# Kernel optimization log

Measured on AMD Instinct MI355X. Metric: run time of the kernel, lower is better.

The kernel has to match this reference:

```python
import jax, jax.numpy as jnp
import numpy as np
from jax import lax

B, H, W = 8, 500, 500
M = 2048          # per-image cap on active bottleneck voxels (ragged -> fixed)
GRID = 125        # bottleneck grid size
ENC_RANGE = 125.0
HEADS, ATTN_CH, CH = 4, 128, 64
EPS = 1e-5
NEG = -1e9

def _conv(x, w, b, stride, pad):
    y = lax.conv_general_dilated(x, w, (stride, stride), pad,
                                 dimension_numbers=('NCHW', 'HWIO', 'NCHW'))
    return y + b[None, :, None, None]

def _maxpool2(m):
    return lax.reduce_window(m, -jnp.inf, lax.max, (1, 1, 2, 2), (1, 1, 2, 2), 'VALID')

def setup_inputs():
    key = jax.random.key(0)
    ks = jax.random.split(key, 12)
    occ = (jax.random.uniform(ks[0], (B, 1, H, W)) < 0.005).astype(jnp.float32)
    x = jax.random.normal(ks[1], (B, 1, H, W), dtype=jnp.float32) * occ
    def rn(k, shape, scale):
        return jax.random.normal(k, shape, dtype=jnp.float32) * scale
    return {
        'x': x,
        'w0': rn(ks[2], (3, 3, 1, 32), 0.3), 'b0': jnp.zeros(32, jnp.float32),
        'g0': jnp.ones(32, jnp.float32), 'be0': jnp.zeros(32, jnp.float32),
        'w1': rn(ks[3], (2, 2, 32, 64), 0.1), 'b1': jnp.zeros(64, jnp.float32),
        'g1': jnp.ones(64, jnp.float32), 'be1': jnp.zeros(64, jnp.float32),
        'w2': rn(ks[4], (2, 2, 64, 64), 0.08), 'b2': jnp.zeros(64, jnp.float32),
        'g2': jnp.ones(64, jnp.float32), 'be2': jnp.zeros(64, jnp.float32),
        'wpe': rn(ks[5], (2, 2, CH), 0.5), 'bpe': jnp.zeros((2, CH), jnp.float32),
        'wq': rn(ks[6], (2, CH, ATTN_CH), 0.12), 'bq': jnp.zeros((2, ATTN_CH), jnp.float32),
        'wk': rn(ks[7], (2, CH, ATTN_CH), 0.12), 'bk': jnp.zeros((2, ATTN_CH), jnp.float32),
        'wv': rn(ks[8], (2, CH, ATTN_CH), 0.12), 'bv': jnp.zeros((2, ATTN_CH), jnp.float32),
        'wo': rn(ks[9], (2, ATTN_CH, CH), 0.09), 'bo': jnp.zeros((2, CH), jnp.float32),
        'wh': rn(ks[10], (CH, 4), 0.12), 'bh': jnp.zeros(4, jnp.float32),
    }

def reference(x, w0, b0, g0, be0, w1, b1, g1, be1, w2, b2, g2, be2,
              wpe, bpe, wq, bq, wk, bk, wv, bv, wo, bo, wh, bh):
    # active-site mask (Voxels.from_dense)
    mask0 = (x != 0).any(axis=1, keepdims=True).astype(x.dtype)   # [B,1,500,500]

    def bn_relu(y, g, be):
        # eval-mode BatchNorm1d over active voxel features (running stats 0/1)
        return jax.nn.relu(g[None, :, None, None] * y / jnp.sqrt(1.0 + EPS)
                           + be[None, :, None, None])

    # enc0: submanifold 3x3/s1 -> active set unchanged; inactive inputs are zero
    y = bn_relu(_conv(x, w0, b0, 1, 'SAME'), g0, be0) * mask0
    # enc1/enc2: strided 2x2/s2 -> output active iff any input in window active
    mask1 = _maxpool2(mask0)
    y = bn_relu(_conv(y, w1, b1, 2, 'VALID'), g1, be1) * mask1
    mask2 = _maxpool2(mask1)
    y = bn_relu(_conv(y, w2, b2, 2, 'VALID'), g2, be2) * mask2    # [B,64,125,125]

    # gather active bottleneck voxels per image (ragged -> fixed M + validity mask)
    mflat = mask2.reshape(B, GRID * GRID)
    vals, idx = lax.top_k(mflat, M)     # active-first; stable tie-break (lowest idx)
    valid = vals                        # [B,M] in {0,1}
    feats = jnp.take_along_axis(
        y.reshape(B, CH, GRID * GRID).transpose(0, 2, 1),
        idx[:, :, None], axis=1)        # [B,M,64]
    pos = jnp.stack([idx // GRID, idx % GRID], axis=-1).astype(x.dtype) / ENC_RANGE

    dh = ATTN_CH // HEADS
    kmask = (1.0 - valid)[:, None, None, :] * NEG
    for i in range(2):  # N_ATTN structurally distinct layers
        pe = pos @ wpe[i] + bpe[i]
        h = feats + pe
        q = (h @ wq[i] + bq[i]).reshape(B, M, HEADS, dh)
        k = (h @ wk[i] + bk[i]).reshape(B, M, HEADS, dh)
        v = (h @ wv[i] + bv[i]).reshape(B, M, HEADS, dh)
        s = jnp.einsum('bqhd,bkhd->bhqk', q, k) / jnp.sqrt(jnp.asarray(dh, x.dtype))
        a = jax.nn.softmax(s + kmask, axis=-1)
        o = jnp.einsum('bhqk,bkhd->bqhd', a, v).reshape(B, M, ATTN_CH)
        feats = (feats + o @ wo[i] + bo[i]) * valid[..., None]

    # sparse_global_avg_pool: mean over active voxels per image
    counts = jnp.clip(valid.sum(axis=1, keepdims=True), 1.0, None)
    pooled = feats.sum(axis=1) / counts                            # [B,64]
    return pooled @ wh + bh                                        # [B,4]
```

## Files before the change

kernel.cpp:

```cpp
#include <hip/hip_runtime.h>

#define BDIM   8
#define NPIX   250000
#define G1N    62500
#define G2N    15625
#define NB0    977
#define NB1    245
#define NB2    62
#define NBALL  (NB0 + NB1 + NB2)
#define CAP0   4096
#define CAP1   4096
#define CAPM   2048
#define CH     64
#define ACH    128
#define NHEADS 4
#define DH     32
#define KSPLIT 4

static constexpr float BN_INV = 0.99999500003749969f;
static constexpr float SCALE2 = 0.25505654734044769f;

typedef _Float16 f16x8 __attribute__((ext_vector_type(8)));
typedef __fp16 h16x2 __attribute__((ext_vector_type(2)));
typedef float f32x4 __attribute__((ext_vector_type(4)));

static constexpr size_t E_MAP0  = 0;
static constexpr size_t E_MAP1  = E_MAP0 + (size_t)BDIM*NPIX;
static constexpr size_t E_CNT   = E_MAP1 + (size_t)BDIM*G1N;
static constexpr size_t E_ZEND  = E_CNT + 32;
static constexpr size_t E_BC    = E_ZEND;
static constexpr size_t E_BO    = E_BC + (size_t)3*BDIM*1024;
static constexpr size_t E_BM    = E_BO + (size_t)3*BDIM*1024;
static constexpr size_t E_LIST0 = E_BM + (size_t)3*BDIM*1024*8;
static constexpr size_t E_LIST1 = E_LIST0 + (size_t)BDIM*CAP0;
static constexpr size_t E_LIST2 = E_LIST1 + (size_t)BDIM*CAP1;
static constexpr size_t E_Y0    = E_LIST2 + (size_t)BDIM*CAPM;
static constexpr size_t E_Y1    = E_Y0 + (size_t)BDIM*CAP0*32;
static constexpr size_t E_FE    = E_Y1 + (size_t)BDIM*CAP1*64;
static constexpr size_t E_QF    = E_FE + (size_t)BDIM*CAPM*64;
static constexpr size_t E_KF    = E_QF + (size_t)32*CAPM*32/2;
static constexpr size_t E_VT    = E_KF + (size_t)32*CAPM*32/2;
static constexpr size_t E_O     = E_VT + (size_t)32*CAPM*32/2;


__global__ __launch_bounds__(256) void k_cntA(const float* __restrict__ x,
                                              int* __restrict__ bcnt,
                                              unsigned long long* __restrict__ bm) {
  int bx = blockIdx.x, b = blockIdx.y, tid = threadIdx.x;
  int level, blk;
  bool act = false;
  if (bx < NB0) {
    level = 0; blk = bx;
    int idx = blk * 256 + tid;
    act = (idx < NPIX) && (x[(size_t)b * NPIX + idx] != 0.f);
  } else if (bx < NB0 + NB1) {
    level = 1; blk = bx - NB0;
    int p = blk * 256 + tid;
    if (p < G1N) {
      int i = p / 250, j = p - i * 250;
      const float* px = x + (size_t)b * NPIX + (2 * i) * 500 + 2 * j;
      act = (px[0] != 0.f) | (px[1] != 0.f) | (px[500] != 0.f) | (px[501] != 0.f);
    }
  } else {
    level = 2; blk = bx - NB0 - NB1;
    int p = blk * 256 + tid;
    if (p < G2N) {
      int i = p / 125, j = p - i * 125;
      const float* px = x + (size_t)b * NPIX + (4 * i) * 500 + 4 * j;
      bool a = false;
#pragma unroll
      for (int r = 0; r < 4; ++r)
#pragma unroll
        for (int c = 0; c < 4; ++c) a |= (px[r * 500 + c] != 0.f);
      act = a;
    }
  }
  unsigned long long mask = __ballot(act);
  size_t mbase = ((size_t)level * BDIM + b) * 1024 + blk;
  __shared__ int wc[4];
  if ((tid & 63) == 0) {
    wc[tid >> 6] = __popcll(mask);
    bm[mbase * 4 + (tid >> 6)] = mask;
  }
  __syncthreads();
  if (tid == 0) bcnt[mbase] = wc[0] + wc[1] + wc[2] + wc[3];
}

__global__ __launch_bounds__(256) void k_emitA(
    const unsigned long long* __restrict__ bm, const int* __restrict__ bcnt,
    int* __restrict__ map0, int* __restrict__ list0,
    int* __restrict__ map1, int* __restrict__ list1,
    int* __restrict__ list2, int* __restrict__ cnt) {
  int bx = blockIdx.x, b = blockIdx.y, tid = threadIdx.x;
  int level, blk, nblk, cbase;
  if (bx < NB0)            { level = 0; blk = bx;             nblk = NB0; cbase = 0; }
  else if (bx < NB0 + NB1) { level = 1; blk = bx - NB0;       nblk = NB1; cbase = BDIM; }
  else                     { level = 2; blk = bx - NB0 - NB1; nblk = NB2; cbase = 2 * BDIM; }
  size_t mbase = ((size_t)level * BDIM + b) * 1024;
  int lane = tid & 63, wv = tid >> 6;
  unsigned long long mask = bm[(mbase + blk) * 4 + wv];
  const int* bc = bcnt + mbase;
  int pre = 0;
  for (int k = tid; k < blk; k += 256) pre += bc[k];
#pragma unroll
  for (int off = 1; off < 64; off <<= 1) pre += __shfl_xor(pre, off);
  __shared__ int wred[4], wbase[4];
  if (lane == 0) { wred[wv] = pre; wbase[wv] = __popcll(mask); }
  __syncthreads();
  if (tid == 0) {
    int s = wred[0] + wred[1] + wred[2] + wred[3];
    for (int w = 0; w < 4; ++w) { int c = wbase[w]; wbase[w] = s; s += c; }
    if (blk == nblk - 1) cnt[cbase + b] = s;
  }
  __syncthreads();
  bool act = (mask >> lane) & 1;
  int slot = wbase[wv] + __popcll(mask & ((1ull << lane) - 1ull));
  int idx = blk * 256 + tid;
  if (level == 0) {
    if (act && slot < CAP0) {
      list0[b * CAP0 + slot] = idx;
      map0[(size_t)b * NPIX + idx] = slot + 1;
    }
  } else if (level == 1) {
    if (act && slot < CAP1) {
      list1[b * CAP1 + slot] = idx;
      map1[(size_t)b * G1N + idx] = slot + 1;
    }
  } else {
    if (act && slot < CAPM) list2[b * CAPM + slot] = idx;
  }
}


__global__ void k_y0(const float* __restrict__ x, const float* __restrict__ w0,
                     const float* __restrict__ b0, const float* __restrict__ g0,
                     const float* __restrict__ be0,
                     const int* __restrict__ list0, const int* __restrict__ cnt,
                     float* __restrict__ y0) {
  int t = blockIdx.x * 256 + threadIdx.x;
  int b = t >> 17;
  int r = t & 131071;
  int slot = r >> 5, c = r & 31;
  int n = min(cnt[b], CAP0);
  if (slot >= n) return;
  int pix = list0[b * CAP0 + slot];
  int i = pix / 500, j = pix - i * 500;
  float acc = b0[c];
#pragma unroll
  for (int di = 0; di < 3; ++di) {
    int ii = i + di - 1;
    if ((unsigned)ii >= 500u) continue;
#pragma unroll
    for (int dj = 0; dj < 3; ++dj) {
      int jj = j + dj - 1;
      if ((unsigned)jj >= 500u) continue;
      acc += x[(size_t)b * NPIX + ii * 500 + jj] * w0[(di * 3 + dj) * 32 + c];
    }
  }
  float o = g0[c] * acc * BN_INV + be0[c];
  y0[((size_t)(b * CAP0) + slot) * 32 + c] = fmaxf(o, 0.f);
}

__global__ __launch_bounds__(256) void k_y1(
    const float* __restrict__ y0, const float* __restrict__ w1,
    const float* __restrict__ b1, const float* __restrict__ g1,
    const float* __restrict__ be1,
    const int* __restrict__ map0, const int* __restrict__ list1,
    const int* __restrict__ cnt, float* __restrict__ y1) {
  int b = blockIdx.x & 7;
  int qblk = blockIdx.x >> 3;
  int sub = threadIdx.x >> 6;
  int co = threadIdx.x & 63;
  int n = min(cnt[BDIM + b], CAP1);
  if (qblk * 32 >= n) return;
  int s0 = qblk * 32 + sub * 8;
  __shared__ float inT[4][4][32][8];
  for (int idx = co; idx < 1024; idx += 64) {
    int s = idx & 7;
    int r = idx >> 3;
    int ci = r & 31, pp = r >> 5;
    float v = 0.f;
    int sg = s0 + s;
    if (sg < n) {
      int p = list1[b * CAP1 + sg];
      int i = p / 250, j = p - i * 250;
      int sm = map0[(size_t)b * NPIX + (2 * i + (pp >> 1)) * 500 + (2 * j + (pp & 1))];
      if (sm) v = y0[((size_t)(b * CAP0) + (sm - 1)) * 32 + ci];
    }
    inT[sub][pp][ci][s] = v;
  }
  __syncthreads();
  float acc[8];
#pragma unroll
  for (int s = 0; s < 8; ++s) acc[s] = b1[co];
#pragma unroll 2
  for (int pp = 0; pp < 4; ++pp)
    for (int ci = 0; ci < 32; ++ci) {
      float wv = w1[((pp << 5) + ci) * 64 + co];
      float4 i0 = *(const float4*)&inT[sub][pp][ci][0];
      float4 i1 = *(const float4*)&inT[sub][pp][ci][4];
      acc[0] += i0.x * wv; acc[1] += i0.y * wv; acc[2] += i0.z * wv; acc[3] += i0.w * wv;
      acc[4] += i1.x * wv; acc[5] += i1.y * wv; acc[6] += i1.z * wv; acc[7] += i1.w * wv;
    }
  int smax = min(8, n - s0);
  for (int s = 0; s < smax; ++s) {
    float o = g1[co] * acc[s] * BN_INV + be1[co];
    y1[((size_t)(b * CAP1) + s0 + s) * 64 + co] = fmaxf(o, 0.f);
  }
}

__global__ __launch_bounds__(256) void k_y2(
    const float* __restrict__ y1, const float* __restrict__ w2,
    const float* __restrict__ b2, const float* __restrict__ g2,
    const float* __restrict__ be2,
    const int* __restrict__ map1, const int* __restrict__ list2,
    const int* __restrict__ cnt, float* __restrict__ feats) {
  int b = blockIdx.x & 7;
  int qblk = blockIdx.x >> 3;
  int sub = threadIdx.x >> 6;
  int co = threadIdx.x & 63;
  int n = min(cnt[2 * BDIM + b], CAPM);
  if (qblk * 32 >= n) return;
  int s0 = qblk * 32 + sub * 8;
  __shared__ float inT[4][4][64][8];
  for (int idx = co; idx < 2048; idx += 64) {
    int s = idx & 7;
    int r = idx >> 3;
    int ci = r & 63, pp = r >> 6;
    float v = 0.f;
    int sg = s0 + s;
    if (sg < n) {
      int p = list2[b * CAPM + sg];
      int i = p / 125, j = p - i * 125;
      int sm = map1[(size_t)b * G1N + (2 * i + (pp >> 1)) * 250 + (2 * j + (pp & 1))];
      if (sm) v = y1[((size_t)(b * CAP1) + (sm - 1)) * 64 + ci];
    }
    inT[sub][pp][ci][s] = v;
  }
  __syncthreads();
  float acc[8];
#pragma unroll
  for (int s = 0; s < 8; ++s) acc[s] = b2[co];
#pragma unroll 2
  for (int pp = 0; pp < 4; ++pp)
    for (int ci = 0; ci < 64; ++ci) {
      float wv = w2[((pp << 6) + ci) * 64 + co];
      float4 i0 = *(const float4*)&inT[sub][pp][ci][0];
      float4 i1 = *(const float4*)&inT[sub][pp][ci][4];
      acc[0] += i0.x * wv; acc[1] += i0.y * wv; acc[2] += i0.z * wv; acc[3] += i0.w * wv;
      acc[4] += i1.x * wv; acc[5] += i1.y * wv; acc[6] += i1.z * wv; acc[7] += i1.w * wv;
    }
  int smax = min(8, n - s0);
  for (int s = 0; s < smax; ++s) {
    float o = g2[co] * acc[s] * BN_INV + be2[co];
    feats[((size_t)(b * CAPM) + s0 + s) * 64 + co] = fmaxf(o, 0.f);
  }
}


__global__ __launch_bounds__(256) void k_qkv(
    const float* __restrict__ feats, const int* __restrict__ list2,
    const int* __restrict__ cnt,
    const float* __restrict__ wpe, const float* __restrict__ bpe,
    const float* __restrict__ wq, const float* __restrict__ bq,
    const float* __restrict__ wk, const float* __restrict__ bk,
    const float* __restrict__ wv, const float* __restrict__ bv,
    int layer, _Float16* __restrict__ qf, _Float16* __restrict__ kf,
    _Float16* __restrict__ vt) {
  int b = blockIdx.x & 7;
  int qblk = blockIdx.x >> 3;
  int sub = threadIdx.x >> 7;
  int o = threadIdx.x & 127;
  int n = min(cnt[2 * BDIM + b], CAPM);
  if (qblk * 16 >= n) return;
  int s0 = qblk * 16 + sub * 8;
  __shared__ float hT[2][64][8];
  for (int idx = o; idx < 512; idx += 128) {
    int s = idx & 7, c = idx >> 3;
    float hv = 0.f;
    int sg = s0 + s;
    if (sg < n) {
      int p = list2[b * CAPM + sg];
      int i = p / 125, j = p - i * 125;
      hv = feats[((size_t)(b * CAPM) + sg) * 64 + c]
         + (float)i * (1.f / 125.f) * wpe[(layer * 2 + 0) * 64 + c]
         + (float)j * (1.f / 125.f) * wpe[(layer * 2 + 1) * 64 + c]
         + bpe[layer * 64 + c];
    }
    hT[sub][c][s] = hv;
  }
  __syncthreads();
  float accq[8], acck[8], accv[8];
  float bqv = bq[layer * 128 + o], bkv = bk[layer * 128 + o], bvv = bv[layer * 128 + o];
#pragma unroll
  for (int s = 0; s < 8; ++s) { accq[s] = bqv; acck[s] = bkv; accv[s] = bvv; }
  const float* wq_ = wq + (size_t)layer * 64 * 128 + o;
  const float* wk_ = wk + (size_t)layer * 64 * 128 + o;
  const float* wv_ = wv + (size_t)layer * 64 * 128 + o;
  for (int c = 0; c < 64; ++c) {
    float wqv = wq_[c * 128], wkv = wk_[c * 128], wvv = wv_[c * 128];
    float4 h0 = *(const float4*)&hT[sub][c][0];
    float4 h1 = *(const float4*)&hT[sub][c][4];
    float hh[8] = {h0.x, h0.y, h0.z, h0.w, h1.x, h1.y, h1.z, h1.w};
#pragma unroll
    for (int s = 0; s < 8; ++s) {
      accq[s] += hh[s] * wqv; acck[s] += hh[s] * wkv; accv[s] += hh[s] * wvv;
    }
  }
  int hd = o >> 5, d = o & 31;
  size_t bh = (size_t)(b * NHEADS + hd);
  int smax = min(8, n - s0);
  for (int s = 0; s < smax; ++s) {
    size_t rb = (bh * CAPM + s0 + s) * 32 + d;
    qf[rb] = (_Float16)(accq[s] * SCALE2);
    kf[rb] = (_Float16)acck[s];
    vt[(bh * 32 + d) * CAPM + s0 + s] = (_Float16)accv[s];
  }
}


union U4H8 { uint4 u; f16x8 h; };
union PK2  { h16x2 h; unsigned int u; };

__device__ __forceinline__ void ptile(
    f16x8 K0, f16x8 K1, f16x8 K2, f16x8 K3,
    f16x8 V0, f16x8 V1, f16x8 V2, f16x8 V3,
    f16x8 fq, f32x4& acc0, f32x4& acc1, float& m, float& l, bool& first,
    unsigned int* P, int swz, int g, int qr, int n, int T0) {
  f32x4 cm = { -m, -m, -m, -m };
  f32x4 st0 = __builtin_amdgcn_mfma_f32_16x16x32_f16(K0, fq, cm, 0, 0, 0);
  f32x4 st1 = __builtin_amdgcn_mfma_f32_16x16x32_f16(K1, fq, cm, 0, 0, 0);
  f32x4 st2 = __builtin_amdgcn_mfma_f32_16x16x32_f16(K2, fq, cm, 0, 0, 0);
  f32x4 st3 = __builtin_amdgcn_mfma_f32_16x16x32_f16(K3, fq, cm, 0, 0, 0);
  if (T0 + 64 > n) {
#pragma unroll
    for (int r = 0; r < 4; ++r) {
      if (T0 + 4 * g + r >= n)      st0[r] = -1e30f;
      if (T0 + 16 + 4 * g + r >= n) st1[r] = -1e30f;
      if (T0 + 32 + 4 * g + r >= n) st2[r] = -1e30f;
      if (T0 + 48 + 4 * g + r >= n) st3[r] = -1e30f;
    }
  }
  float x0 = fmaxf(fmaxf(st0[0], st0[1]), st0[2]);
  float x1 = fmaxf(fmaxf(st0[3], st1[0]), st1[1]);
  float x2 = fmaxf(fmaxf(st1[2], st1[3]), st2[0]);
  float x3 = fmaxf(fmaxf(st2[1], st2[2]), st2[3]);
  float x4 = fmaxf(fmaxf(st3[0], st3[1]), st3[2]);
  float tm = fmaxf(fmaxf(fmaxf(x0, x1), fmaxf(x2, x3)), fmaxf(x4, st3[3]));
  tm = fmaxf(tm, __shfl_xor(tm, 16));
  tm = fmaxf(tm, __shfl_xor(tm, 32));
  bool gw = first || (__any(tm > 0.f) != 0);
  float d = 0.f;
  if (gw) {
    d = first ? tm : fmaxf(tm, 0.f);
    if (!first) {
      float f_ = exp2f(-d);
      l *= f_;
      acc0 *= f_;
      acc1 *= f_;
    }
    m += d;
    first = false;
  }
  PK2 a0, a1, a2, a3, a4, a5, a6, a7;
  a0.h = __builtin_amdgcn_cvt_pkrtz(exp2f(st0[0] - d), exp2f(st0[1] - d));
  a1.h = __builtin_amdgcn_cvt_pkrtz(exp2f(st0[2] - d), exp2f(st0[3] - d));
  a2.h = __builtin_amdgcn_cvt_pkrtz(exp2f(st1[0] - d), exp2f(st1[1] - d));
  a3.h = __builtin_amdgcn_cvt_pkrtz(exp2f(st1[2] - d), exp2f(st1[3] - d));
  a4.h = __builtin_amdgcn_cvt_pkrtz(exp2f(st2[0] - d), exp2f(st2[1] - d));
  a5.h = __builtin_amdgcn_cvt_pkrtz(exp2f(st2[2] - d), exp2f(st2[3] - d));
  a6.h = __builtin_amdgcn_cvt_pkrtz(exp2f(st3[0] - d), exp2f(st3[1] - d));
  a7.h = __builtin_amdgcn_cvt_pkrtz(exp2f(st3[2] - d), exp2f(st3[3] - d));
  h16x2 one2 = { (__fp16)1.f, (__fp16)1.f };
  float ls = 0.f;
  ls = __builtin_amdgcn_fdot2(a0.h, one2, ls, false);
  ls = __builtin_amdgcn_fdot2(a1.h, one2, ls, false);
  ls = __builtin_amdgcn_fdot2(a2.h, one2, ls, false);
  ls = __builtin_amdgcn_fdot2(a3.h, one2, ls, false);
  ls = __builtin_amdgcn_fdot2(a4.h, one2, ls, false);
  ls = __builtin_amdgcn_fdot2(a5.h, one2, ls, false);
  ls = __builtin_amdgcn_fdot2(a6.h, one2, ls, false);
  ls = __builtin_amdgcn_fdot2(a7.h, one2, ls, false);
  l += ls;
  P[(qr * 32 + 0 + 2 * g) ^ swz] = a0.u;
  P[(qr * 32 + 1 + 2 * g) ^ swz] = a1.u;
  P[(qr * 32 + 8 + 2 * g) ^ swz] = a2.u;
  P[(qr * 32 + 9 + 2 * g) ^ swz] = a3.u;
  P[(qr * 32 + 16 + 2 * g) ^ swz] = a4.u;
  P[(qr * 32 + 17 + 2 * g) ^ swz] = a5.u;
  P[(qr * 32 + 24 + 2 * g) ^ swz] = a6.u;
  P[(qr * 32 + 25 + 2 * g) ^ swz] = a7.u;
  __builtin_amdgcn_sched_barrier(0);
  U4H8 pa0, pa1;
  pa0.u = *(const uint4*)&P[(qr * 32 + 4 * g) ^ swz];
  pa1.u = *(const uint4*)&P[(qr * 32 + 16 + 4 * g) ^ swz];
  acc0 = __builtin_amdgcn_mfma_f32_16x16x32_f16(V0, pa0.h, acc0, 0, 0, 0);
  acc1 = __builtin_amdgcn_mfma_f32_16x16x32_f16(V1, pa0.h, acc1, 0, 0, 0);
  acc0 = __builtin_amdgcn_mfma_f32_16x16x32_f16(V2, pa1.h, acc0, 0, 0, 0);
  acc1 = __builtin_amdgcn_mfma_f32_16x16x32_f16(V3, pa1.h, acc1, 0, 0, 0);
}

#define LOADK(K0, K1, K2, K3, T0)                                          \
  K0 = *(const f16x8*)(kf + (bh + (T0) + qr) * 32 + g8);                   \
  K1 = *(const f16x8*)(kf + (bh + (T0) + 16 + qr) * 32 + g8);              \
  K2 = *(const f16x8*)(kf + (bh + (T0) + 32 + qr) * 32 + g8);              \
  K3 = *(const f16x8*)(kf + (bh + (T0) + 48 + qr) * 32 + g8);

#define LOADV(V0, V1, V2, V3, T0)                                          \
  V0 = *(const f16x8*)(vbase + (size_t)qr * CAPM + (T0) + g8);             \
  V1 = *(const f16x8*)(vbase + (size_t)(16 + qr) * CAPM + (T0) + g8);      \
  V2 = *(const f16x8*)(vbase + (size_t)qr * CAPM + (T0) + 32 + g8);        \
  V3 = *(const f16x8*)(vbase + (size_t)(16 + qr) * CAPM + (T0) + 32 + g8);

__global__ __launch_bounds__(256) void k_attn(
    const _Float16* __restrict__ qf, const _Float16* __restrict__ kf,
    const _Float16* __restrict__ vt, const int* __restrict__ cnt,
    _Float16* __restrict__ obuf) {
  int b  = blockIdx.x & 7;
  int rr = blockIdx.x >> 3;
  int qt = rr & 127;
  int h  = rr >> 7;
  int n = min(cnt[2 * BDIM + b], CAPM);
  int q0 = qt * 16;
  if (q0 >= n) return;
  int ks = threadIdx.x >> 6;
  int lane = threadIdx.x & 63;
  int g = lane >> 4, qr = lane & 15;
  int g8 = g * 8;
  size_t bh = (size_t)(b * NHEADS + h) * CAPM;
  const _Float16* vbase = vt + (size_t)(b * NHEADS + h) * 32 * CAPM;
  f16x8 fq = *(const f16x8*)(qf + (bh + q0 + qr) * 32 + g8);
  f32x4 acc0 = {0.f, 0.f, 0.f, 0.f}, acc1 = {0.f, 0.f, 0.f, 0.f};
  float m = 0.f, l = 0.f;
  bool first = true;
  __shared__ unsigned int P4[4][512];
  __shared__ float partA[4][16][33];
  __shared__ float mlA[4][16][2];
  unsigned int* P = P4[ks];
  int swz = (qr & 7) << 2;

  int nt = (n + 63) >> 6;
  int tpc = (nt + KSPLIT - 1) / KSPLIT;
  int tb = ks * tpc, te = min(nt, tb + tpc);
  if (tb < te) {
    f16x8 ka0, ka1, ka2, ka3, va0, va1, va2, va3;
    f16x8 kb0, kb1, kb2, kb3, vb0, vb1, vb2, vb3;
    LOADK(ka0, ka1, ka2, ka3, tb * 64)
    LOADV(va0, va1, va2, va3, tb * 64)
    for (int t = tb; t < te; t += 2) {
      if (t + 1 < te) {
        LOADK(kb0, kb1, kb2, kb3, (t + 1) * 64)
        LOADV(vb0, vb1, vb2, vb3, (t + 1) * 64)
      }
      ptile(ka0, ka1, ka2, ka3, va0, va1, va2, va3, fq, acc0, acc1, m, l,
            first, P, swz, g, qr, n, t * 64);
      if (t + 1 < te) {
        if (t + 2 < te) {
          LOADK(ka0, ka1, ka2, ka3, (t + 2) * 64)
          LOADV(va0, va1, va2, va3, (t + 2) * 64)
        }
        ptile(kb0, kb1, kb2, kb3, vb0, vb1, vb2, vb3, fq, acc0, acc1, m, l,
              first, P, swz, g, qr, n, (t + 1) * 64);
      }
    }
  }
  l += __shfl_xor(l, 16);
  l += __shfl_xor(l, 32);
#pragma unroll
  for (int r = 0; r < 4; ++r) {
    partA[ks][qr][4 * g + r] = acc0[r];
    partA[ks][qr][16 + 4 * g + r] = acc1[r];
  }
  if (g == 0) { mlA[ks][qr][0] = first ? -1e30f : m; mlA[ks][qr][1] = l; }
  __syncthreads();
  int t = threadIdx.x;
  int s = t >> 4;
  int c0 = (t & 15) * 2;
  int tok = q0 + s;
  if (tok < n) {
    float m0 = mlA[0][s][0], l0 = mlA[0][s][1];
    float m1 = mlA[1][s][0], l1 = mlA[1][s][1];
    float m2 = mlA[2][s][0], l2 = mlA[2][s][1];
    float m3 = mlA[3][s][0], l3 = mlA[3][s][1];
    float M = fmaxf(fmaxf(m0, m1), fmaxf(m2, m3));
    float w0_ = exp2f(m0 - M), w1_ = exp2f(m1 - M);
    float w2_ = exp2f(m2 - M), w3_ = exp2f(m3 - M);
    float invL = 1.f / (w0_ * l0 + w1_ * l1 + w2_ * l2 + w3_ * l3);
    float v0 = (partA[0][s][c0] * w0_ + partA[1][s][c0] * w1_ +
                partA[2][s][c0] * w2_ + partA[3][s][c0] * w3_) * invL;
    float v1 = (partA[0][s][c0 + 1] * w0_ + partA[1][s][c0 + 1] * w1_ +
                partA[2][s][c0 + 1] * w2_ + partA[3][s][c0 + 1] * w3_) * invL;
    _Float16* op = obuf + ((size_t)b * CAPM + tok) * ACH + h * DH;
    op[c0] = (_Float16)v0;
    op[c0 + 1] = (_Float16)v1;
  }
}


__global__ __launch_bounds__(256) void k_proj(
    const _Float16* __restrict__ obuf, const float* __restrict__ wo,
    const float* __restrict__ bo, const int* __restrict__ cnt,
    int layer, float* __restrict__ feats) {
  int b = blockIdx.x & 7;
  int sblk = blockIdx.x >> 3;
  int s0 = sblk * 4;
  int n = min(cnt[2 * BDIM + b], CAPM);
  if (s0 >= n) return;
  __shared__ float oT[128][4];
  int t = threadIdx.x;
#pragma unroll
  for (int k = 0; k < 2; ++k) {
    int id = t + k * 256;
    int c = id >> 2, s = id & 3;
    int sg = s0 + s;
    oT[c][s] = (sg < n) ? (float)obuf[((size_t)b * CAPM + sg) * ACH + c] : 0.f;
  }
  __syncthreads();
  int s = t >> 6, co = t & 63;
  float acc = bo[layer * 64 + co];
  const float* w = wo + (size_t)layer * 128 * 64 + co;
#pragma unroll 8
  for (int c = 0; c < 128; ++c) acc += oT[c][s] * w[c * 64];
  int tok = s0 + s;
  if (tok < n) feats[((size_t)(b * CAPM) + tok) * 64 + co] += acc;
}


__global__ __launch_bounds__(1024) void k_head(
    const float* __restrict__ feats, const float* __restrict__ wh,
    const float* __restrict__ bhd, const int* __restrict__ cnt,
    float* __restrict__ out) {
  int b = blockIdx.x;
  int n = min(cnt[2 * BDIM + b], CAPM);
  int c = threadIdx.x & 63, chunk = threadIdx.x >> 6;
  int lo = chunk * 128, hi = min(n, lo + 128);
  float s = 0.f;
  for (int mm = lo; mm < hi; ++mm)
    s += feats[((size_t)(b * CAPM) + mm) * 64 + c];
  __shared__ float red[16][64];
  __shared__ float pooled[64];
  red[chunk][c] = s;
  __syncthreads();
  if (threadIdx.x < 64) {
    float tot = 0.f;
#pragma unroll
    for (int k = 0; k < 16; ++k) tot += red[k][c];
    pooled[c] = tot / (float)max(n, 1);
  }
  __syncthreads();
  if (threadIdx.x < 4) {
    float o = bhd[threadIdx.x];
#pragma unroll
    for (int c2 = 0; c2 < 64; ++c2) o += pooled[c2] * wh[c2 * 4 + threadIdx.x];
    out[b * 4 + threadIdx.x] = o;
  }
}


extern "C" void kernel_launch(void* const* d_in, const int* in_sizes, int n_in,
                              void* d_out, int out_size, void* d_ws, size_t ws_size,
                              hipStream_t stream) {
  const float* x   = (const float*)d_in[0];
  const float* w0  = (const float*)d_in[1];
  const float* b0  = (const float*)d_in[2];
  const float* g0  = (const float*)d_in[3];
  const float* be0 = (const float*)d_in[4];
  const float* w1  = (const float*)d_in[5];
  const float* b1  = (const float*)d_in[6];
  const float* g1  = (const float*)d_in[7];
  const float* be1 = (const float*)d_in[8];
  const float* w2  = (const float*)d_in[9];
  const float* b2  = (const float*)d_in[10];
  const float* g2  = (const float*)d_in[11];
  const float* be2 = (const float*)d_in[12];
  const float* wpe = (const float*)d_in[13];
  const float* bpe = (const float*)d_in[14];
  const float* wq  = (const float*)d_in[15];
  const float* bq  = (const float*)d_in[16];
  const float* wk  = (const float*)d_in[17];
  const float* bk  = (const float*)d_in[18];
  const float* wv  = (const float*)d_in[19];
  const float* bv  = (const float*)d_in[20];
  const float* wo  = (const float*)d_in[21];
  const float* bo  = (const float*)d_in[22];
  const float* wh  = (const float*)d_in[23];
  const float* bh  = (const float*)d_in[24];

  int* wsI = (int*)d_ws;
  float* wsF = (float*)d_ws;
  unsigned long long* bm = (unsigned long long*)(wsI + E_BM);
  _Float16* qf = (_Float16*)(wsI + E_QF);
  _Float16* kf = (_Float16*)(wsI + E_KF);
  _Float16* vt = (_Float16*)(wsI + E_VT);
  _Float16* ob = (_Float16*)(wsI + E_O);

  hipMemsetAsync(d_ws, 0, E_ZEND * 4, stream);

  k_cntA<<<dim3(NBALL, BDIM), 256, 0, stream>>>(x, wsI + E_BC, bm);
  k_emitA<<<dim3(NBALL, BDIM), 256, 0, stream>>>(
      bm, wsI + E_BC, wsI + E_MAP0, wsI + E_LIST0, wsI + E_MAP1, wsI + E_LIST1,
      wsI + E_LIST2, wsI + E_CNT);

  k_y0<<<(BDIM * CAP0 * 32) / 256, 256, 0, stream>>>(
      x, w0, b0, g0, be0, wsI + E_LIST0, wsI + E_CNT, wsF + E_Y0);
  k_y1<<<BDIM * (CAP1 / 32), 256, 0, stream>>>(
      wsF + E_Y0, w1, b1, g1, be1, wsI + E_MAP0, wsI + E_LIST1, wsI + E_CNT, wsF + E_Y1);
  k_y2<<<BDIM * (CAPM / 32), 256, 0, stream>>>(
      wsF + E_Y1, w2, b2, g2, be2, wsI + E_MAP1, wsI + E_LIST2, wsI + E_CNT, wsF + E_FE);

  for (int layer = 0; layer < 2; ++layer) {
    k_qkv<<<BDIM * (CAPM / 16), 256, 0, stream>>>(
        wsF + E_FE, wsI + E_LIST2, wsI + E_CNT, wpe, bpe, wq, bq, wk, bk, wv, bv,
        layer, qf, kf, vt);
    k_attn<<<BDIM * NHEADS * (CAPM / 16), 256, 0, stream>>>(
        qf, kf, vt, wsI + E_CNT, ob);
    k_proj<<<BDIM * (CAPM / 4), 256, 0, stream>>>(
        ob, wo, bo, wsI + E_CNT, layer, wsF + E_FE);
  }

  k_head<<<BDIM, 1024, 0, stream>>>(wsF + E_FE, wh, bh, wsI + E_CNT, (float*)d_out);
}
```

Baseline: 239.1 us.

## Software-pipeline QK^T MFMAs one tile ahead of softmax in attention kernel

Splits the per-tile attention step into a QK^T stage and a softmax/PV stage. The loop now issues the score MFMAs for the next key tile before running the exp/rowsum/PV work of the current one, so matrix-core latency can overlap with VALU work. It also reworks the online-softmax bookkeeping: the max starts at -1e30 and is subtracted explicitly instead of being folded into the MFMA accumulator, and the `first` flag and a sched_barrier are removed. The price is more live score registers, which may raise register pressure.

```diff
diff --git a/kernel.cpp b/kernel.cpp
--- a/kernel.cpp
+++ b/kernel.cpp
@@ -322,84 +322,6 @@
 union U4H8 { uint4 u; f16x8 h; };
 union PK2  { h16x2 h; unsigned int u; };
 
-__device__ __forceinline__ void ptile(
-    f16x8 K0, f16x8 K1, f16x8 K2, f16x8 K3,
-    f16x8 V0, f16x8 V1, f16x8 V2, f16x8 V3,
-    f16x8 fq, f32x4& acc0, f32x4& acc1, float& m, float& l, bool& first,
-    unsigned int* P, int swz, int g, int qr, int n, int T0) {
-  f32x4 cm = { -m, -m, -m, -m };
-  f32x4 st0 = __builtin_amdgcn_mfma_f32_16x16x32_f16(K0, fq, cm, 0, 0, 0);
-  f32x4 st1 = __builtin_amdgcn_mfma_f32_16x16x32_f16(K1, fq, cm, 0, 0, 0);
-  f32x4 st2 = __builtin_amdgcn_mfma_f32_16x16x32_f16(K2, fq, cm, 0, 0, 0);
-  f32x4 st3 = __builtin_amdgcn_mfma_f32_16x16x32_f16(K3, fq, cm, 0, 0, 0);
-  if (T0 + 64 > n) {
-#pragma unroll
-    for (int r = 0; r < 4; ++r) {
-      if (T0 + 4 * g + r >= n)      st0[r] = -1e30f;
-      if (T0 + 16 + 4 * g + r >= n) st1[r] = -1e30f;
-      if (T0 + 32 + 4 * g + r >= n) st2[r] = -1e30f;
-      if (T0 + 48 + 4 * g + r >= n) st3[r] = -1e30f;
-    }
-  }
-  float x0 = fmaxf(fmaxf(st0[0], st0[1]), st0[2]);
-  float x1 = fmaxf(fmaxf(st0[3], st1[0]), st1[1]);
-  float x2 = fmaxf(fmaxf(st1[2], st1[3]), st2[0]);
-  float x3 = fmaxf(fmaxf(st2[1], st2[2]), st2[3]);
-  float x4 = fmaxf(fmaxf(st3[0], st3[1]), st3[2]);
-  float tm = fmaxf(fmaxf(fmaxf(x0, x1), fmaxf(x2, x3)), fmaxf(x4, st3[3]));
-  tm = fmaxf(tm, __shfl_xor(tm, 16));
-  tm = fmaxf(tm, __shfl_xor(tm, 32));
-  bool gw = first || (__any(tm > 0.f) != 0);
-  float d = 0.f;
-  if (gw) {
-    d = first ? tm : fmaxf(tm, 0.f);
-    if (!first) {
-      float f_ = exp2f(-d);
-      l *= f_;
-      acc0 *= f_;
-      acc1 *= f_;
-    }
-    m += d;
-    first = false;
-  }
-  PK2 a0, a1, a2, a3, a4, a5, a6, a7;
-  a0.h = __builtin_amdgcn_cvt_pkrtz(exp2f(st0[0] - d), exp2f(st0[1] - d));
-  a1.h = __builtin_amdgcn_cvt_pkrtz(exp2f(st0[2] - d), exp2f(st0[3] - d));
-  a2.h = __builtin_amdgcn_cvt_pkrtz(exp2f(st1[0] - d), exp2f(st1[1] - d));
-  a3.h = __builtin_amdgcn_cvt_pkrtz(exp2f(st1[2] - d), exp2f(st1[3] - d));
-  a4.h = __builtin_amdgcn_cvt_pkrtz(exp2f(st2[0] - d), exp2f(st2[1] - d));
-  a5.h = __builtin_amdgcn_cvt_pkrtz(exp2f(st2[2] - d), exp2f(st2[3] - d));
-  a6.h = __builtin_amdgcn_cvt_pkrtz(exp2f(st3[0] - d), exp2f(st3[1] - d));
-  a7.h = __builtin_amdgcn_cvt_pkrtz(exp2f(st3[2] - d), exp2f(st3[3] - d));
-  h16x2 one2 = { (__fp16)1.f, (__fp16)1.f };
-  float ls = 0.f;
-  ls = __builtin_amdgcn_fdot2(a0.h, one2, ls, false);
-  ls = __builtin_amdgcn_fdot2(a1.h, one2, ls, false);
-  ls = __builtin_amdgcn_fdot2(a2.h, one2, ls, false);
-  ls = __builtin_amdgcn_fdot2(a3.h, one2, ls, false);
-  ls = __builtin_amdgcn_fdot2(a4.h, one2, ls, false);
-  ls = __builtin_amdgcn_fdot2(a5.h, one2, ls, false);
-  ls = __builtin_amdgcn_fdot2(a6.h, one2, ls, false);
-  ls = __builtin_amdgcn_fdot2(a7.h, one2, ls, false);
-  l += ls;
-  P[(qr * 32 + 0 + 2 * g) ^ swz] = a0.u;
-  P[(qr * 32 + 1 + 2 * g) ^ swz] = a1.u;
-  P[(qr * 32 + 8 + 2 * g) ^ swz] = a2.u;
-  P[(qr * 32 + 9 + 2 * g) ^ swz] = a3.u;
-  P[(qr * 32 + 16 + 2 * g) ^ swz] = a4.u;
-  P[(qr * 32 + 17 + 2 * g) ^ swz] = a5.u;
-  P[(qr * 32 + 24 + 2 * g) ^ swz] = a6.u;
-  P[(qr * 32 + 25 + 2 * g) ^ swz] = a7.u;
-  __builtin_amdgcn_sched_barrier(0);
-  U4H8 pa0, pa1;
-  pa0.u = *(const uint4*)&P[(qr * 32 + 4 * g) ^ swz];
-  pa1.u = *(const uint4*)&P[(qr * 32 + 16 + 4 * g) ^ swz];
-  acc0 = __builtin_amdgcn_mfma_f32_16x16x32_f16(V0, pa0.h, acc0, 0, 0, 0);
-  acc1 = __builtin_amdgcn_mfma_f32_16x16x32_f16(V1, pa0.h, acc1, 0, 0, 0);
-  acc0 = __builtin_amdgcn_mfma_f32_16x16x32_f16(V2, pa1.h, acc0, 0, 0, 0);
-  acc1 = __builtin_amdgcn_mfma_f32_16x16x32_f16(V3, pa1.h, acc1, 0, 0, 0);
-}
-
 #define LOADK(K0, K1, K2, K3, T0)                                          \
   K0 = *(const f16x8*)(kf + (bh + (T0) + qr) * 32 + g8);                   \
   K1 = *(const f16x8*)(kf + (bh + (T0) + 16 + qr) * 32 + g8);              \
@@ -411,6 +333,78 @@
   V1 = *(const f16x8*)(vbase + (size_t)(16 + qr) * CAPM + (T0) + g8);      \
   V2 = *(const f16x8*)(vbase + (size_t)qr * CAPM + (T0) + 32 + g8);        \
   V3 = *(const f16x8*)(vbase + (size_t)(16 + qr) * CAPM + (T0) + 32 + g8);
+
+#define QKT(K0, K1, K2, K3, S0, S1, S2, S3, T0)                            \
+  {                                                                        \
+    f32x4 z = {0.f, 0.f, 0.f, 0.f};                                        \
+    S0 = __builtin_amdgcn_mfma_f32_16x16x32_f16(K0, fq, z, 0, 0, 0);       \
+    S1 = __builtin_amdgcn_mfma_f32_16x16x32_f16(K1, fq, z, 0, 0, 0);       \
+    S2 = __builtin_amdgcn_mfma_f32_16x16x32_f16(K2, fq, z, 0, 0, 0);       \
+    S3 = __builtin_amdgcn_mfma_f32_16x16x32_f16(K3, fq, z, 0, 0, 0);       \
+    if ((T0) + 64 > n) {                                                   \
+      _Pragma("unroll") for (int r = 0; r < 4; ++r) {                      \
+        if ((T0) + 4 * g + r >= n)      S0[r] = -1e30f;                    \
+        if ((T0) + 16 + 4 * g + r >= n) S1[r] = -1e30f;                    \
+        if ((T0) + 32 + 4 * g + r >= n) S2[r] = -1e30f;                    \
+        if ((T0) + 48 + 4 * g + r >= n) S3[r] = -1e30f;                    \
+      }                                                                    \
+    }                                                                      \
+  }
+
+#define SVT(S0, S1, S2, S3, V0, V1, V2, V3)                                \
+  {                                                                        \
+    float x0 = fmaxf(fmaxf(S0[0], S0[1]), S0[2]);                          \
+    float x1 = fmaxf(fmaxf(S0[3], S1[0]), S1[1]);                          \
+    float x2 = fmaxf(fmaxf(S1[2], S1[3]), S2[0]);                          \
+    float x3 = fmaxf(fmaxf(S2[1], S2[2]), S2[3]);                          \
+    float x4 = fmaxf(fmaxf(S3[0], S3[1]), S3[2]);                          \
+    float tm = fmaxf(fmaxf(fmaxf(x0, x1), fmaxf(x2, x3)), fmaxf(x4, S3[3]));\
+    tm = fmaxf(tm, __shfl_xor(tm, 16));                                    \
+    tm = fmaxf(tm, __shfl_xor(tm, 32));                                    \
+    if (__any(tm > m)) {                                                   \
+      float mn = fmaxf(m, tm);                                             \
+      float f_ = exp2f(m - mn);                                            \
+      m = mn;                                                              \
+      l *= f_;                                                             \
+      acc0 *= f_;                                                          \
+      acc1 *= f_;                                                          \
+    }                                                                      \
+    PK2 a0, a1, a2, a3, a4, a5, a6, a7;                                    \
+    a0.h = __builtin_amdgcn_cvt_pkrtz(exp2f(S0[0] - m), exp2f(S0[1] - m)); \
+    a1.h = __builtin_amdgcn_cvt_pkrtz(exp2f(S0[2] - m), exp2f(S0[3] - m)); \
+    a2.h = __builtin_amdgcn_cvt_pkrtz(exp2f(S1[0] - m), exp2f(S1[1] - m)); \
+    a3.h = __builtin_amdgcn_cvt_pkrtz(exp2f(S1[2] - m), exp2f(S1[3] - m)); \
+    a4.h = __builtin_amdgcn_cvt_pkrtz(exp2f(S2[0] - m), exp2f(S2[1] - m)); \
+    a5.h = __builtin_amdgcn_cvt_pkrtz(exp2f(S2[2] - m), exp2f(S2[3] - m)); \
+    a6.h = __builtin_amdgcn_cvt_pkrtz(exp2f(S3[0] - m), exp2f(S3[1] - m)); \
+    a7.h = __builtin_amdgcn_cvt_pkrtz(exp2f(S3[2] - m), exp2f(S3[3] - m)); \
+    h16x2 one2 = { (__fp16)1.f, (__fp16)1.f };                             \
+    float ls = 0.f;                                                        \
+    ls = __builtin_amdgcn_fdot2(a0.h, one2, ls, false);                    \
+    ls = __builtin_amdgcn_fdot2(a1.h, one2, ls, false);                    \
+    ls = __builtin_amdgcn_fdot2(a2.h, one2, ls, false);                    \
+    ls = __builtin_amdgcn_fdot2(a3.h, one2, ls, false);                    \
+    ls = __builtin_amdgcn_fdot2(a4.h, one2, ls, false);                    \
+    ls = __builtin_amdgcn_fdot2(a5.h, one2, ls, false);                    \
+    ls = __builtin_amdgcn_fdot2(a6.h, one2, ls, false);                    \
+    ls = __builtin_amdgcn_fdot2(a7.h, one2, ls, false);                    \
+    l += ls;                                                               \
+    P[(qr * 32 + 0 + 2 * g) ^ swz] = a0.u;                                 \
+    P[(qr * 32 + 1 + 2 * g) ^ swz] = a1.u;                                 \
+    P[(qr * 32 + 8 + 2 * g) ^ swz] = a2.u;                                 \
+    P[(qr * 32 + 9 + 2 * g) ^ swz] = a3.u;                                 \
+    P[(qr * 32 + 16 + 2 * g) ^ swz] = a4.u;                                \
+    P[(qr * 32 + 17 + 2 * g) ^ swz] = a5.u;                                \
+    P[(qr * 32 + 24 + 2 * g) ^ swz] = a6.u;                                \
+    P[(qr * 32 + 25 + 2 * g) ^ swz] = a7.u;                                \
+    U4H8 pa0, pa1;                                                         \
+    pa0.u = *(const uint4*)&P[(qr * 32 + 4 * g) ^ swz];                    \
+    pa1.u = *(const uint4*)&P[(qr * 32 + 16 + 4 * g) ^ swz];               \
+    acc0 = __builtin_amdgcn_mfma_f32_16x16x32_f16(V0, pa0.h, acc0, 0, 0, 0);\
+    acc1 = __builtin_amdgcn_mfma_f32_16x16x32_f16(V1, pa0.h, acc1, 0, 0, 0);\
+    acc0 = __builtin_amdgcn_mfma_f32_16x16x32_f16(V2, pa1.h, acc0, 0, 0, 0);\
+    acc1 = __builtin_amdgcn_mfma_f32_16x16x32_f16(V3, pa1.h, acc1, 0, 0, 0);\
+  }
 
 __global__ __launch_bounds__(256) void k_attn(
     const _Float16* __restrict__ qf, const _Float16* __restrict__ kf,
@@ -431,8 +425,7 @@
   const _Float16* vbase = vt + (size_t)(b * NHEADS + h) * 32 * CAPM;
   f16x8 fq = *(const f16x8*)(qf + (bh + q0 + qr) * 32 + g8);
   f32x4 acc0 = {0.f, 0.f, 0.f, 0.f}, acc1 = {0.f, 0.f, 0.f, 0.f};
-  float m = 0.f, l = 0.f;
-  bool first = true;
+  float m = -1e30f, l = 0.f;
   __shared__ unsigned int P4[4][512];
   __shared__ float partA[4][16][33];
   __shared__ float mlA[4][16][2];
@@ -445,22 +438,28 @@
   if (tb < te) {
     f16x8 ka0, ka1, ka2, ka3, va0, va1, va2, va3;
     f16x8 kb0, kb1, kb2, kb3, vb0, vb1, vb2, vb3;
+    f32x4 sA0, sA1, sA2, sA3, sB0, sB1, sB2, sB3;
     LOADK(ka0, ka1, ka2, ka3, tb * 64)
     LOADV(va0, va1, va2, va3, tb * 64)
+    if (tb + 1 < te) {
+      LOADK(kb0, kb1, kb2, kb3, (tb + 1) * 64)
+      LOADV(vb0, vb1, vb2, vb3, (tb + 1) * 64)
+    }
+    QKT(ka0, ka1, ka2, ka3, sA0, sA1, sA2, sA3, tb * 64)
     for (int t = tb; t < te; t += 2) {
+      if (t + 1 < te) QKT(kb0, kb1, kb2, kb3, sB0, sB1, sB2, sB3, (t + 1) * 64)
+      SVT(sA0, sA1, sA2, sA3, va0, va1, va2, va3)
+      if (t + 2 < te) {
+        LOADK(ka0, ka1, ka2, ka3, (t + 2) * 64)
+        LOADV(va0, va1, va2, va3, (t + 2) * 64)
+      }
       if (t + 1 < te) {
-        LOADK(kb0, kb1, kb2, kb3, (t + 1) * 64)
-        LOADV(vb0, vb1, vb2, vb3, (t + 1) * 64)
-      }
-      ptile(ka0, ka1, ka2, ka3, va0, va1, va2, va3, fq, acc0, acc1, m, l,
-            first, P, swz, g, qr, n, t * 64);
-      if (t + 1 < te) {
-        if (t + 2 < te) {
-          LOADK(ka0, ka1, ka2, ka3, (t + 2) * 64)
-          LOADV(va0, va1, va2, va3, (t + 2) * 64)
+        SVT(sB0, sB1, sB2, sB3, vb0, vb1, vb2, vb3)
+        if (t + 3 < te) {
+          LOADK(kb0, kb1, kb2, kb3, (t + 3) * 64)
+          LOADV(vb0, vb1, vb2, vb3, (t + 3) * 64)
         }
-        ptile(kb0, kb1, kb2, kb3, vb0, vb1, vb2, vb3, fq, acc0, acc1, m, l,
-              first, P, swz, g, qr, n, (t + 1) * 64);
+        if (t + 2 < te) QKT(ka0, ka1, ka2, ka3, sA0, sA1, sA2, sA3, (t + 2) * 64)
       }
     }
   }
@@ -471,7 +470,7 @@
     partA[ks][qr][4 * g + r] = acc0[r];
     partA[ks][qr][16 + 4 * g + r] = acc1[r];
   }
-  if (g == 0) { mlA[ks][qr][0] = first ? -1e30f : m; mlA[ks][qr][1] = l; }
+  if (g == 0) { mlA[ks][qr][0] = m; mlA[ks][qr][1] = l; }
   __syncthreads();
   int t = threadIdx.x;
   int s = t >> 4;
```

New measurement: 241.8 us. No clear change (+1.1%).
